# Optimization experiments

Measured on AMD Instinct MI355X. Metric: run time of the kernel, lower is better.

The kernel has to match this reference:

```python
import jax, jax.numpy as jnp
import numpy as np

D_MODEL = 1024
NUM_HEADS = 16
HEAD_DIM = D_MODEL // NUM_HEADS


def setup_inputs() -> dict:
    key = jax.random.key(0)
    ks = jax.random.split(key, 9)
    s = D_MODEL ** -0.5  # roughly like nn.Linear init scale
    x = jax.random.normal(ks[0], (4, 2048, D_MODEL), dtype=jnp.float32)
    Wq = jax.random.normal(ks[1], (D_MODEL, D_MODEL), dtype=jnp.float32) * s
    bq = jax.random.normal(ks[2], (D_MODEL,), dtype=jnp.float32) * s
    Wk = jax.random.normal(ks[3], (D_MODEL, D_MODEL), dtype=jnp.float32) * s
    bk = jax.random.normal(ks[4], (D_MODEL,), dtype=jnp.float32) * s
    Wv = jax.random.normal(ks[5], (D_MODEL, D_MODEL), dtype=jnp.float32) * s
    bv = jax.random.normal(ks[6], (D_MODEL,), dtype=jnp.float32) * s
    Wo = jax.random.normal(ks[7], (D_MODEL, D_MODEL), dtype=jnp.float32) * s
    bo = jax.random.normal(ks[8], (D_MODEL,), dtype=jnp.float32) * s
    return {"x": x, "Wq": Wq, "bq": bq, "Wk": Wk, "bk": bk,
            "Wv": Wv, "bv": bv, "Wo": Wo, "bo": bo}


def reference(x, Wq, bq, Wk, bk, Wv, bv, Wo, bo):
    B, S, D = x.shape
    H, Dh = NUM_HEADS, HEAD_DIM
    scale = Dh ** -0.5
    # nn.Linear: x @ W.T + b
    q = (x @ Wq.T + bq).reshape(B, S, H, Dh)
    k = (x @ Wk.T + bk).reshape(B, S, H, Dh)
    v = (x @ Wv.T + bv).reshape(B, S, H, Dh)
    # scores: (B, H, S, S), full materialization as in the original bmm path
    dp = scale * jnp.einsum('bqhd,bkhd->bhqk', q, k)
    att = jax.nn.softmax(dp, axis=-1)
    out = jnp.einsum('bhqk,bkhd->bqhd', att, v).reshape(B, S, D)
    return out @ Wo.T + bo
```

## Files before the change

kernel.cpp:

```cpp
#include <hip/hip_runtime.h>
#include <stdint.h>

typedef __attribute__((ext_vector_type(8))) __bf16 bf16x8;
typedef __attribute__((ext_vector_type(4))) float floatx4;

#define DEV __device__ __forceinline__

DEV unsigned short f2bf(float f) {
    union { float f; unsigned u; } uf; uf.f = f;
    unsigned u = uf.u;
    unsigned r = (u + 0x7fffu + ((u >> 16) & 1u)) >> 16;
    return (unsigned short)r;
}

DEV float fast_exp2(float x) {
#if __has_builtin(__builtin_amdgcn_exp2f)
    return __builtin_amdgcn_exp2f(x);
#else
    return exp2f(x);
#endif
}

DEV unsigned pack_trunc2(float lo, float hi) {
    return __builtin_amdgcn_perm(__float_as_uint(hi), __float_as_uint(lo), 0x07060302u);
}

DEV void async16(const void* g, void* l) {
    __builtin_amdgcn_global_load_lds(
        (const __attribute__((address_space(1))) void*)g,
        (__attribute__((address_space(3))) void*)l, 16, 0, 0);
}

__global__ void cast_all_kernel(const float* __restrict__ x,
                                const float* __restrict__ Wq, const float* __restrict__ Wk,
                                const float* __restrict__ Wv, const float* __restrict__ Wo,
                                const float* __restrict__ bq, const float* __restrict__ bk,
                                const float* __restrict__ bv,
                                unsigned short* __restrict__ xb,
                                unsigned short* __restrict__ wqkv,
                                unsigned short* __restrict__ wo,
                                float* __restrict__ bqkv) {
    const int NX = 2097152;
    const int NW = 262144;
    int i = blockIdx.x * blockDim.x + threadIdx.x;
    if (i < NX) {
        float4 v = reinterpret_cast<const float4*>(x)[i];
        ushort4 o;
        o.x = f2bf(v.x); o.y = f2bf(v.y); o.z = f2bf(v.z); o.w = f2bf(v.w);
        reinterpret_cast<ushort4*>(xb)[i] = o;
        return;
    }
    int j = i - NX;
    if (j < 4 * NW) {
        int seg = j >> 18, off = j & (NW - 1);
        const float* src = (seg == 0) ? Wq : (seg == 1) ? Wk : (seg == 2) ? Wv : Wo;
        unsigned short* dst = (seg < 3) ? (wqkv + seg * 1048576) : wo;
        float4 v = reinterpret_cast<const float4*>(src)[off];
        ushort4 o;
        o.x = f2bf(v.x); o.y = f2bf(v.y); o.z = f2bf(v.z); o.w = f2bf(v.w);
        reinterpret_cast<ushort4*>(dst)[off] = o;
        return;
    }
    int k = j - 4 * NW;
    if (k < 768) {
        int seg = k >> 8, off = k & 255;
        const float* src = (seg == 0) ? bq : (seg == 1) ? bk : bv;
        reinterpret_cast<float4*>(bqkv)[k] = reinterpret_cast<const float4*>(src)[off];
    }
}

template <int MODE>
__global__ __launch_bounds__(256)
void gemm128(const unsigned short* __restrict__ A,
             const unsigned short* __restrict__ B,
             const float* __restrict__ bias,
             unsigned short* __restrict__ q_ws,
             unsigned short* __restrict__ k_ws,
             unsigned short* __restrict__ v_ws,
             float* __restrict__ fout) {
    constexpr int K = 1024;
    __shared__ alignas(16) unsigned short smem[128 * 136];
    unsigned short* sA = smem;
    unsigned short* sB = smem + 128 * 64;
    unsigned short* sT = smem;

    const int tid = threadIdx.x;
    const int w = tid >> 6, lane = tid & 63, quad = lane >> 4, l16 = lane & 15;
    const int wr = w >> 1, wc = w & 1;
    const int bm = blockIdx.x, bn = blockIdx.y;
    const int arow0 = bm * 128, brow0 = bn * 128;

    floatx4 acc[4][4];
#pragma unroll
    for (int i = 0; i < 4; i++)
#pragma unroll
        for (int j = 0; j < 4; j++) acc[i][j] = (floatx4){0.f, 0.f, 0.f, 0.f};

    for (int k0 = 0; k0 < K; k0 += 64) {
#pragma unroll
        for (int i = 0; i < 4; i++) {
            int cb = i * 256 + w * 64;
            int ci = cb + lane;
            int row = ci >> 3, cl = ci & 7, cs = cl ^ (row & 7);
            async16(A + (size_t)(arow0 + row) * K + k0 + cs * 8, (char*)sA + cb * 16);
            async16(B + (size_t)(brow0 + row) * K + k0 + cs * 8, (char*)sB + cb * 16);
        }
        __syncthreads();
#pragma unroll
        for (int kk = 0; kk < 2; kk++) {
            bf16x8 aF[4], bF[4];
#pragma unroll
            for (int i = 0; i < 4; i++) {
                int row = wr * 64 + i * 16 + l16;
                int c = kk * 4 + quad, ph = c ^ (row & 7);
                aF[i] = *reinterpret_cast<const bf16x8*>(sA + row * 64 + ph * 8);
            }
#pragma unroll
            for (int j = 0; j < 4; j++) {
                int row = wc * 64 + j * 16 + l16;
                int c = kk * 4 + quad, ph = c ^ (row & 7);
                bF[j] = *reinterpret_cast<const bf16x8*>(sB + row * 64 + ph * 8);
            }
#pragma unroll
            for (int i = 0; i < 4; i++)
#pragma unroll
                for (int j = 0; j < 4; j++)
                    acc[i][j] = __builtin_amdgcn_mfma_f32_16x16x32_bf16(
                        aF[i], bF[j], acc[i][j], 0, 0, 0);
        }
        __syncthreads();
    }

    if (bn < 16) {
        unsigned short* dst = (bn < 8) ? q_ws : k_ws;
        const float sc = (bn < 8) ? 0.18033688f : 1.0f;
#pragma unroll
        for (int j = 0; j < 4; j++) {
            const int c = wc * 64 + j * 16 + l16;
            const float bia = bias[brow0 + c];
#pragma unroll
            for (int i = 0; i < 4; i++) {
                int s_loc = wr * 64 + i * 16 + quad * 4;
#pragma unroll
                for (int r = 0; r < 4; r++)
                    sT[(s_loc + r) * 136 + c] = f2bf((acc[i][j][r] + bia) * sc);
            }
        }
        __syncthreads();
        const int nnbase = (bn & 7) * 128;
        const int c0 = (tid & 15) * 8;
        const int h = (nnbase + c0) >> 6, d = c0 & 63;
#pragma unroll
        for (int it = 0; it < 8; it++) {
            int s_loc = (tid >> 4) + it * 16;
            int s = arow0 + s_loc;
            int bb = s >> 11, s4 = s & 2047;
            uint4 vdat = *reinterpret_cast<const uint4*>(sT + s_loc * 136 + c0);
            *reinterpret_cast<uint4*>(
                dst + ((size_t)(bb * 16 + h) * 2048 + s4) * 64 + d) = vdat;
        }
    } else {
#pragma unroll
        for (int j = 0; j < 4; j++) {
            const int c = wc * 64 + j * 16 + l16;
            const float bia = bias[brow0 + c];
#pragma unroll
            for (int i = 0; i < 4; i++) {
#pragma unroll
                for (int r = 0; r < 4; r++) {
                    int v = wr * 64 + (quad * 4 + r) * 4 + i;
                    sT[c * 136 + v] = f2bf(acc[i][j][r] + bia);
                }
            }
        }
        __syncthreads();
        const int bb = bm >> 4, blk = bm & 15;
        const int chunk = tid & 15;
#pragma unroll
        for (int it = 0; it < 8; it++) {
            int row = (tid >> 4) + it * 16;
            int h = (bn - 16) * 2 + (row >> 6), d = row & 63;
            ushort4 lo = *reinterpret_cast<const ushort4*>(sT + row * 136 + chunk * 8);
            ushort4 hi = *reinterpret_cast<const ushort4*>(sT + row * 136 + chunk * 8 + 4);
            size_t off = ((size_t)(bb * 16 + h) * 64 + d) * 2048 + blk * 128 + chunk * 8;
            *reinterpret_cast<ushort4*>(v_ws + off) = lo;
            *reinterpret_cast<ushort4*>(v_ws + off + 4) = hi;
        }
    }
}

__global__ __launch_bounds__(256)
void gemm_oproj(const unsigned short* __restrict__ A,
                const unsigned short* __restrict__ Bw,
                const float* __restrict__ bias,
                float* __restrict__ fout) {
    constexpr int K = 1024;
    __shared__ alignas(16) unsigned short smem[192 * 64];
    unsigned short* sA = smem;
    unsigned short* sB = smem + 128 * 64;
    float* sT32 = reinterpret_cast<float*>(smem);

    const int tid = threadIdx.x;
    const int w = tid >> 6, lane = tid & 63, quad = lane >> 4, l16 = lane & 15;
    const int wr = w >> 1, wc = w & 1;
    const int bm = blockIdx.x, bn = blockIdx.y;
    const int arow0 = bm * 128, brow0 = bn * 64;

    floatx4 acc[4][2];
#pragma unroll
    for (int i = 0; i < 4; i++)
#pragma unroll
        for (int j = 0; j < 2; j++) acc[i][j] = (floatx4){0.f, 0.f, 0.f, 0.f};

    for (int k0 = 0; k0 < K; k0 += 64) {
#pragma unroll
        for (int i = 0; i < 4; i++) {
            int ci = i * 256 + tid;
            int row = ci >> 3, cs = (ci & 7) ^ (row & 7);
            async16(A + (size_t)(arow0 + row) * K + k0 + cs * 8, (char*)sA + ci * 16);
        }
#pragma unroll
        for (int i = 0; i < 2; i++) {
            int ci = i * 256 + tid;
            int row = ci >> 3, cs = (ci & 7) ^ (row & 7);
            async16(Bw + (size_t)(brow0 + row) * K + k0 + cs * 8, (char*)sB + ci * 16);
        }
        __syncthreads();
#pragma unroll
        for (int kk = 0; kk < 2; kk++) {
            bf16x8 aF[4], bF[2];
#pragma unroll
            for (int i = 0; i < 4; i++) {
                int row = wr * 64 + i * 16 + l16;
                int ph = (kk * 4 + quad) ^ (row & 7);
                aF[i] = *reinterpret_cast<const bf16x8*>(sA + row * 64 + ph * 8);
            }
#pragma unroll
            for (int j = 0; j < 2; j++) {
                int row = wc * 32 + j * 16 + l16;
                int ph = (kk * 4 + quad) ^ (row & 7);
                bF[j] = *reinterpret_cast<const bf16x8*>(sB + row * 64 + ph * 8);
            }
#pragma unroll
            for (int i = 0; i < 4; i++)
#pragma unroll
                for (int j = 0; j < 2; j++)
                    acc[i][j] = __builtin_amdgcn_mfma_f32_16x16x32_bf16(
                        aF[i], bF[j], acc[i][j], 0, 0, 0);
        }
        __syncthreads();
    }

#pragma unroll
    for (int ch = 0; ch < 2; ch++) {
        if (ch) __syncthreads();
        if (wr == ch) {
#pragma unroll
            for (int j = 0; j < 2; j++) {
                const int c = wc * 32 + j * 16 + l16;
                const float bia = bias[brow0 + c];
#pragma unroll
                for (int i = 0; i < 4; i++) {
                    int s_loc = i * 16 + quad * 4;
#pragma unroll
                    for (int r = 0; r < 4; r++)
                        sT32[(s_loc + r) * 68 + c] = acc[i][j][r] + bia;
                }
            }
        }
        __syncthreads();
        const int cpos = (tid & 15) * 4;
#pragma unroll
        for (int it = 0; it < 4; it++) {
            int s_loc = (tid >> 4) + it * 16;
            int grow = arow0 + ch * 64 + s_loc;
            float4 vv = *reinterpret_cast<const float4*>(sT32 + s_loc * 68 + cpos);
            *reinterpret_cast<float4*>(fout + (size_t)grow * 1024 + brow0 + cpos) = vv;
        }
    }
}

__global__ __launch_bounds__(256, 4)
void attn_kernel(const unsigned short* __restrict__ q_ws,
                 const unsigned short* __restrict__ k_ws,
                 const unsigned short* __restrict__ v_ws,
                 unsigned short* __restrict__ o_ws) {
    __shared__ alignas(16) unsigned short smem[20480];

    const int tid = threadIdx.x;
    const int w = tid >> 6, lane = tid & 63, quad = lane >> 4, l16 = lane & 15;
    const int id = blockIdx.x;
    const int bh = (id >> 7) * 8 + (id & 7);
    const int q0 = ((id >> 3) & 15) * 128;
    const size_t base = (size_t)bh * 2048 * 64;

    unsigned short* sPw = smem + 16384 + w * 1024;

    bf16x8 aQ[2][2];
#pragma unroll
    for (int g = 0; g < 2; g++) {
        int qrow = q0 + g * 64 + w * 16 + l16;
        const unsigned short* qp = q_ws + base + (size_t)qrow * 64 + quad * 8;
        aQ[g][0] = *reinterpret_cast<const bf16x8*>(qp);
        aQ[g][1] = *reinterpret_cast<const bf16x8*>(qp + 32);
    }

    const unsigned short* kg[2];
    const unsigned short* vg[2];
    int loff[2];
#pragma unroll
    for (int it = 0; it < 2; it++) {
        int ci = it * 256 + tid;
        int row = ci >> 3, cl = ci & 7, cs = cl ^ (row & 7);
        kg[it] = k_ws + base + (size_t)row * 64 + cs * 8;
        vg[it] = v_ws + base + (size_t)row * 2048 + cs * 8;
        loff[it] = ci * 8;
    }

    const __bf16 one = (__bf16)1.0f;
    const bf16x8 vOnes = {one, one, one, one, one, one, one, one};

    floatx4 oAcc[2][4], rsAcc[2];
#pragma unroll
    for (int g = 0; g < 2; g++) {
#pragma unroll
        for (int j = 0; j < 4; j++) oAcc[g][j] = (floatx4){0.f, 0.f, 0.f, 0.f};
        rsAcc[g] = (floatx4){0.f, 0.f, 0.f, 0.f};
    }

    {
#pragma unroll
        for (int it = 0; it < 2; it++) {
            async16(kg[it], smem + loff[it]);
            async16(vg[it], smem + 8192 + loff[it]);
        }
    }

    const int xr = l16 & 7;
    const int offw0 = l16 * 64 + (((2 * quad) ^ xr) << 3);
    const int offw1 = l16 * 64 + (((2 * quad + 1) ^ xr) << 3);
    const int offr0 = l16 * 64 + ((quad ^ xr) << 3);
    const int offr1 = l16 * 64 + (((4 + quad) ^ xr) << 3);

    for (int t = 0; t < 32; t++) {
        const int b = t & 1;
        const unsigned short* sK = smem + b * 4096;
        const unsigned short* sVt = smem + 8192 + b * 4096;
        __syncthreads();

        if (t < 31) {
            const int kv0 = (t + 1) * 64;
            unsigned short* dK = smem + (b ^ 1) * 4096;
            unsigned short* dV = smem + 8192 + (b ^ 1) * 4096;
#pragma unroll
            for (int it = 0; it < 2; it++) {
                async16(kg[it] + (size_t)kv0 * 64, dK + loff[it]);
                async16(vg[it] + kv0, dV + loff[it]);
            }
        }

        floatx4 s0[4], s1[4];
#pragma unroll
        for (int j = 0; j < 4; j++) {
            s0[j] = (floatx4){0.f, 0.f, 0.f, 0.f};
            s1[j] = (floatx4){0.f, 0.f, 0.f, 0.f};
        }
#pragma unroll
        for (int kk = 0; kk < 2; kk++) {
#pragma unroll
            for (int j = 0; j < 4; j++) {
                int krow = j * 16 + l16;
                int ph = (kk * 4 + quad) ^ (krow & 7);
                bf16x8 aK = *reinterpret_cast<const bf16x8*>(sK + krow * 64 + ph * 8);
                s0[j] = __builtin_amdgcn_mfma_f32_16x16x32_bf16(aK, aQ[0][kk], s0[j], 0, 0, 0);
                s1[j] = __builtin_amdgcn_mfma_f32_16x16x32_bf16(aK, aQ[1][kk], s1[j], 0, 0, 0);
            }
        }

#pragma unroll
        for (int j = 0; j < 4; j++)
#pragma unroll
            for (int r = 0; r < 4; r++) s0[j][r] = fast_exp2(s0[j][r]);
        {
            uint4 w0, w1;
            w0.x = pack_trunc2(s0[0][0], s0[1][0]);
            w0.y = pack_trunc2(s0[2][0], s0[3][0]);
            w0.z = pack_trunc2(s0[0][1], s0[1][1]);
            w0.w = pack_trunc2(s0[2][1], s0[3][1]);
            w1.x = pack_trunc2(s0[0][2], s0[1][2]);
            w1.y = pack_trunc2(s0[2][2], s0[3][2]);
            w1.z = pack_trunc2(s0[0][3], s0[1][3]);
            w1.w = pack_trunc2(s0[2][3], s0[3][3]);
            *reinterpret_cast<uint4*>(sPw + offw0) = w0;
            *reinterpret_cast<uint4*>(sPw + offw1) = w1;
        }

#pragma unroll
        for (int j = 0; j < 4; j++)
#pragma unroll
            for (int r = 0; r < 4; r++) s1[j][r] = fast_exp2(s1[j][r]);

        asm volatile("s_waitcnt lgkmcnt(0)" ::: "memory");
        __builtin_amdgcn_sched_barrier(0);

        {
            bf16x8 aPa = *reinterpret_cast<const bf16x8*>(sPw + offr0);
            bf16x8 aPb = *reinterpret_cast<const bf16x8*>(sPw + offr1);
#pragma unroll
            for (int jd = 0; jd < 4; jd++) {
                int drow = jd * 16 + l16;
                int ph0 = quad ^ (drow & 7);
                bf16x8 bVa = *reinterpret_cast<const bf16x8*>(sVt + drow * 64 + ph0 * 8);
                oAcc[0][jd] = __builtin_amdgcn_mfma_f32_16x16x32_bf16(aPa, bVa, oAcc[0][jd], 0, 0, 0);
                int ph1 = (4 + quad) ^ (drow & 7);
                bf16x8 bVb = *reinterpret_cast<const bf16x8*>(sVt + drow * 64 + ph1 * 8);
                oAcc[0][jd] = __builtin_amdgcn_mfma_f32_16x16x32_bf16(aPb, bVb, oAcc[0][jd], 0, 0, 0);
            }
            rsAcc[0] = __builtin_amdgcn_mfma_f32_16x16x32_bf16(aPa, vOnes, rsAcc[0], 0, 0, 0);
            rsAcc[0] = __builtin_amdgcn_mfma_f32_16x16x32_bf16(aPb, vOnes, rsAcc[0], 0, 0, 0);
        }

        {
            uint4 w0, w1;
            w0.x = pack_trunc2(s1[0][0], s1[1][0]);
            w0.y = pack_trunc2(s1[2][0], s1[3][0]);
            w0.z = pack_trunc2(s1[0][1], s1[1][1]);
            w0.w = pack_trunc2(s1[2][1], s1[3][1]);
            w1.x = pack_trunc2(s1[0][2], s1[1][2]);
            w1.y = pack_trunc2(s1[2][2], s1[3][2]);
            w1.z = pack_trunc2(s1[0][3], s1[1][3]);
            w1.w = pack_trunc2(s1[2][3], s1[3][3]);
            *reinterpret_cast<uint4*>(sPw + offw0) = w0;
            *reinterpret_cast<uint4*>(sPw + offw1) = w1;
        }

        asm volatile("s_waitcnt lgkmcnt(0)" ::: "memory");
        __builtin_amdgcn_sched_barrier(0);

        {
            bf16x8 aPa = *reinterpret_cast<const bf16x8*>(sPw + offr0);
            bf16x8 aPb = *reinterpret_cast<const bf16x8*>(sPw + offr1);
#pragma unroll
            for (int jd = 0; jd < 4; jd++) {
                int drow = jd * 16 + l16;
                int ph0 = quad ^ (drow & 7);
                bf16x8 bVa = *reinterpret_cast<const bf16x8*>(sVt + drow * 64 + ph0 * 8);
                oAcc[1][jd] = __builtin_amdgcn_mfma_f32_16x16x32_bf16(aPa, bVa, oAcc[1][jd], 0, 0, 0);
                int ph1 = (4 + quad) ^ (drow & 7);
                bf16x8 bVb = *reinterpret_cast<const bf16x8*>(sVt + drow * 64 + ph1 * 8);
                oAcc[1][jd] = __builtin_amdgcn_mfma_f32_16x16x32_bf16(aPb, bVb, oAcc[1][jd], 0, 0, 0);
            }
            rsAcc[1] = __builtin_amdgcn_mfma_f32_16x16x32_bf16(aPa, vOnes, rsAcc[1], 0, 0, 0);
            rsAcc[1] = __builtin_amdgcn_mfma_f32_16x16x32_bf16(aPb, vOnes, rsAcc[1], 0, 0, 0);
        }
    }

    const int bb = bh >> 4, h = bh & 15;
#pragma unroll
    for (int g = 0; g < 2; g++) {
        float inv[4];
#pragma unroll
        for (int r = 0; r < 4; r++) inv[r] = 1.0f / rsAcc[g][r];
#pragma unroll
        for (int jd = 0; jd < 4; jd++) {
            int d = jd * 16 + l16;
#pragma unroll
            for (int r = 0; r < 4; r++) {
                int s = q0 + g * 64 + w * 16 + quad * 4 + r;
                float v = oAcc[g][jd][r] * inv[r];
                o_ws[((size_t)bb * 2048 + s) * 1024 + h * 64 + d] = f2bf(v);
            }
        }
    }
}

extern "C" void kernel_launch(void* const* d_in, const int* in_sizes, int n_in,
                              void* d_out, int out_size, void* d_ws, size_t ws_size,
                              hipStream_t stream) {
    const float* x  = (const float*)d_in[0];
    const float* Wq = (const float*)d_in[1];
    const float* bq = (const float*)d_in[2];
    const float* Wk = (const float*)d_in[3];
    const float* bk = (const float*)d_in[4];
    const float* Wv = (const float*)d_in[5];
    const float* bv = (const float*)d_in[6];
    const float* Wo = (const float*)d_in[7];
    const float* bo = (const float*)d_in[8];
    float* out = (float*)d_out;

    char* ws = (char*)d_ws;
    unsigned short* xb   = (unsigned short*)(ws);
    unsigned short* wqkv = (unsigned short*)(ws + (16ull << 20));
    unsigned short* wo   = (unsigned short*)(ws + (22ull << 20));
    float*          bqkv = (float*)(ws + (24ull << 20));
    unsigned short* q_ws = (unsigned short*)(ws + (25ull << 20));
    unsigned short* k_ws = (unsigned short*)(ws + (41ull << 20));
    unsigned short* v_ws = (unsigned short*)(ws + (57ull << 20));
    unsigned short* o_ws = xb;

    cast_all_kernel<<<12291, 256, 0, stream>>>(x, Wq, Wk, Wv, Wo, bq, bk, bv,
                                               xb, wqkv, wo, bqkv);

    gemm128<0><<<dim3(64, 24), 256, 0, stream>>>(xb, wqkv, bqkv, q_ws, k_ws, v_ws, nullptr);
    attn_kernel<<<1024, 256, 0, stream>>>(q_ws, k_ws, v_ws, o_ws);
    gemm_oproj<<<dim3(64, 16), 256, 0, stream>>>(o_ws, wo, bo, out);
}
```

Before: 266.5 us.

## Shrink QKV GEMM shared memory for occupancy and prioritize MFMA waves in attention

The QKV projection GEMM now stages its epilogue transpose in two 64-row halves, with a sync between them. This cuts its shared buffer from 128x136 to 16384 elements, and launch_bounds now requests 5 blocks per CU to raise occupancy. The attention kernel wraps its QK^T and PV MFMA blocks in s_setprio(1)/s_setprio(0) so that waves issuing matrix work get scheduling priority over waves doing exp and packing. The cost is extra barriers in the epilogue and possible register pressure from the occupancy hint.

Result: slower. 363.0 us (+36.2%).

```diff
diff --git a/kernel.cpp b/kernel.cpp
--- a/kernel.cpp
+++ b/kernel.cpp
@@ -70,7 +70,7 @@
 }
 
 template <int MODE>
-__global__ __launch_bounds__(256)
+__global__ __launch_bounds__(256, 5)
 void gemm128(const unsigned short* __restrict__ A,
              const unsigned short* __restrict__ B,
              const float* __restrict__ bias,
@@ -79,7 +79,7 @@
              unsigned short* __restrict__ v_ws,
              float* __restrict__ fout) {
     constexpr int K = 1024;
-    __shared__ alignas(16) unsigned short smem[128 * 136];
+    __shared__ alignas(16) unsigned short smem[16384];
     unsigned short* sA = smem;
     unsigned short* sB = smem + 128 * 64;
     unsigned short* sT = smem;
@@ -134,57 +134,70 @@
     if (bn < 16) {
         unsigned short* dst = (bn < 8) ? q_ws : k_ws;
         const float sc = (bn < 8) ? 0.18033688f : 1.0f;
-#pragma unroll
-        for (int j = 0; j < 4; j++) {
-            const int c = wc * 64 + j * 16 + l16;
-            const float bia = bias[brow0 + c];
-#pragma unroll
-            for (int i = 0; i < 4; i++) {
-                int s_loc = wr * 64 + i * 16 + quad * 4;
-#pragma unroll
-                for (int r = 0; r < 4; r++)
-                    sT[(s_loc + r) * 136 + c] = f2bf((acc[i][j][r] + bia) * sc);
-            }
-        }
-        __syncthreads();
         const int nnbase = (bn & 7) * 128;
         const int c0 = (tid & 15) * 8;
         const int h = (nnbase + c0) >> 6, d = c0 & 63;
 #pragma unroll
-        for (int it = 0; it < 8; it++) {
-            int s_loc = (tid >> 4) + it * 16;
-            int s = arow0 + s_loc;
-            int bb = s >> 11, s4 = s & 2047;
-            uint4 vdat = *reinterpret_cast<const uint4*>(sT + s_loc * 136 + c0);
-            *reinterpret_cast<uint4*>(
-                dst + ((size_t)(bb * 16 + h) * 2048 + s4) * 64 + d) = vdat;
+        for (int ch = 0; ch < 2; ch++) {
+            if (ch) __syncthreads();
+            if (wr == ch) {
+#pragma unroll
+                for (int j = 0; j < 4; j++) {
+                    const int c = wc * 64 + j * 16 + l16;
+                    const float bia = bias[brow0 + c];
+#pragma unroll
+                    for (int i = 0; i < 4; i++) {
+                        int s_loc = i * 16 + quad * 4;
+#pragma unroll
+                        for (int r = 0; r < 4; r++)
+                            sT[(s_loc + r) * 136 + c] = f2bf((acc[i][j][r] + bia) * sc);
+                    }
+                }
+            }
+            __syncthreads();
+#pragma unroll
+            for (int it = 0; it < 4; it++) {
+                int s_loc = (tid >> 4) + it * 16;
+                int s = arow0 + ch * 64 + s_loc;
+                int bb = s >> 11, s4 = s & 2047;
+                uint4 vdat = *reinterpret_cast<const uint4*>(sT + s_loc * 136 + c0);
+                *reinterpret_cast<uint4*>(
+                    dst + ((size_t)(bb * 16 + h) * 2048 + s4) * 64 + d) = vdat;
+            }
         }
     } else {
-#pragma unroll
-        for (int j = 0; j < 4; j++) {
-            const int c = wc * 64 + j * 16 + l16;
-            const float bia = bias[brow0 + c];
-#pragma unroll
-            for (int i = 0; i < 4; i++) {
-#pragma unroll
-                for (int r = 0; r < 4; r++) {
-                    int v = wr * 64 + (quad * 4 + r) * 4 + i;
-                    sT[c * 136 + v] = f2bf(acc[i][j][r] + bia);
+        const int bb2 = bm >> 4, blk = bm & 15;
+        const int chunk = tid & 15;
+#pragma unroll
+        for (int ch = 0; ch < 2; ch++) {
+            if (ch) __syncthreads();
+            if (wc == ch) {
+#pragma unroll
+                for (int j = 0; j < 4; j++) {
+                    const int c = wc * 64 + j * 16 + l16;
+                    const int cl = j * 16 + l16;
+                    const float bia = bias[brow0 + c];
+#pragma unroll
+                    for (int i = 0; i < 4; i++) {
+#pragma unroll
+                        for (int r = 0; r < 4; r++) {
+                            int v = wr * 64 + (quad * 4 + r) * 4 + i;
+                            sT[cl * 136 + v] = f2bf(acc[i][j][r] + bia);
+                        }
+                    }
                 }
             }
-        }
-        __syncthreads();
-        const int bb = bm >> 4, blk = bm & 15;
-        const int chunk = tid & 15;
-#pragma unroll
-        for (int it = 0; it < 8; it++) {
-            int row = (tid >> 4) + it * 16;
-            int h = (bn - 16) * 2 + (row >> 6), d = row & 63;
-            ushort4 lo = *reinterpret_cast<const ushort4*>(sT + row * 136 + chunk * 8);
-            ushort4 hi = *reinterpret_cast<const ushort4*>(sT + row * 136 + chunk * 8 + 4);
-            size_t off = ((size_t)(bb * 16 + h) * 64 + d) * 2048 + blk * 128 + chunk * 8;
-            *reinterpret_cast<ushort4*>(v_ws + off) = lo;
-            *reinterpret_cast<ushort4*>(v_ws + off + 4) = hi;
+            __syncthreads();
+#pragma unroll
+            for (int it = 0; it < 4; it++) {
+                int rl = (tid >> 4) + it * 16;
+                int h2 = (bn - 16) * 2 + ch, d2 = rl;
+                ushort4 lo = *reinterpret_cast<const ushort4*>(sT + rl * 136 + chunk * 8);
+                ushort4 hi = *reinterpret_cast<const ushort4*>(sT + rl * 136 + chunk * 8 + 4);
+                size_t off = ((size_t)(bb2 * 16 + h2) * 64 + d2) * 2048 + blk * 128 + chunk * 8;
+                *reinterpret_cast<ushort4*>(v_ws + off) = lo;
+                *reinterpret_cast<ushort4*>(v_ws + off + 4) = hi;
+            }
         }
     }
 }
@@ -365,6 +378,7 @@
             s0[j] = (floatx4){0.f, 0.f, 0.f, 0.f};
             s1[j] = (floatx4){0.f, 0.f, 0.f, 0.f};
         }
+        __builtin_amdgcn_s_setprio(1);
 #pragma unroll
         for (int kk = 0; kk < 2; kk++) {
 #pragma unroll
@@ -376,6 +390,7 @@
                 s1[j] = __builtin_amdgcn_mfma_f32_16x16x32_bf16(aK, aQ[1][kk], s1[j], 0, 0, 0);
             }
         }
+        __builtin_amdgcn_s_setprio(0);
 
 #pragma unroll
         for (int j = 0; j < 4; j++)
@@ -406,6 +421,7 @@
         {
             bf16x8 aPa = *reinterpret_cast<const bf16x8*>(sPw + offr0);
             bf16x8 aPb = *reinterpret_cast<const bf16x8*>(sPw + offr1);
+            __builtin_amdgcn_s_setprio(1);
 #pragma unroll
             for (int jd = 0; jd < 4; jd++) {
                 int drow = jd * 16 + l16;
@@ -418,6 +434,7 @@
             }
             rsAcc[0] = __builtin_amdgcn_mfma_f32_16x16x32_bf16(aPa, vOnes, rsAcc[0], 0, 0, 0);
             rsAcc[0] = __builtin_amdgcn_mfma_f32_16x16x32_bf16(aPb, vOnes, rsAcc[0], 0, 0, 0);
+            __builtin_amdgcn_s_setprio(0);
         }
 
         {
@@ -440,6 +457,7 @@
         {
             bf16x8 aPa = *reinterpret_cast<const bf16x8*>(sPw + offr0);
             bf16x8 aPb = *reinterpret_cast<const bf16x8*>(sPw + offr1);
+            __builtin_amdgcn_s_setprio(1);
 #pragma unroll
             for (int jd = 0; jd < 4; jd++) {
                 int drow = jd * 16 + l16;
@@ -452,6 +470,7 @@
             }
             rsAcc[1] = __builtin_amdgcn_mfma_f32_16x16x32_bf16(aPa, vOnes, rsAcc[1], 0, 0, 0);
             rsAcc[1] = __builtin_amdgcn_mfma_f32_16x16x32_bf16(aPb, vOnes, rsAcc[1], 0, 0, 0);
+            __builtin_amdgcn_s_setprio(0);
         }
     }
 
```
